# Performance work log

Hardware: AMD Instinct MI355X
Metric: run time of the kernel (lower is better)

The kernel has to match this reference:

```python
import jax, jax.numpy as jnp
import numpy as np

NUM_GROUPS = 32
NUM_HEADS = 8
EPS = 1e-6


def group_norm(x, gamma, beta):
    B, C, H, W = x.shape
    xg = x.reshape(B, NUM_GROUPS, C // NUM_GROUPS, H, W)
    mean = xg.mean(axis=(2, 3, 4), keepdims=True)
    var = xg.var(axis=(2, 3, 4), keepdims=True)
    xn = (xg - mean) * jax.lax.rsqrt(var + EPS)
    xn = xn.reshape(B, C, H, W)
    return xn * gamma[None, :, None, None] + beta[None, :, None, None]


def setup_inputs() -> dict:
    key = jax.random.key(0)
    ks = jax.random.split(key, 3)
    B, C, H, W = 8, 512, 32, 32
    x = jax.random.normal(ks[0], (B, C, H, W), dtype=jnp.float32)
    # xavier_uniform for conv1x1: fan_in=C, fan_out per weight
    lim_qkv = float(np.sqrt(6.0 / (C + 3 * C)))
    w_qkv = jax.random.uniform(ks[1], (3 * C, C), minval=-lim_qkv, maxval=lim_qkv, dtype=jnp.float32)
    b_qkv = jnp.zeros((3 * C,), dtype=jnp.float32)
    lim_p = float(np.sqrt(6.0 / (C + C)))
    w_proj = jax.random.uniform(ks[2], (C, C), minval=-lim_p, maxval=lim_p, dtype=jnp.float32)
    b_proj = jnp.zeros((C,), dtype=jnp.float32)
    gamma = jnp.ones((C,), dtype=jnp.float32)
    beta = jnp.zeros((C,), dtype=jnp.float32)
    return {"x": x, "gamma": gamma, "beta": beta, "w_qkv": w_qkv, "b_qkv": b_qkv,
            "w_proj": w_proj, "b_proj": b_proj}


def reference(x, gamma, beta, w_qkv, b_qkv, w_proj, b_proj):
    B, C, H, W = x.shape
    N = H * W
    hd = C // NUM_HEADS
    scale = hd ** -0.5

    x_norm = group_norm(x, gamma, beta)
    # conv1x1 == channel GEMM: (B,C,H,W) -> (B,3C,H,W)
    qkv = jnp.einsum('bchw,oc->bohw', x_norm, w_qkv) + b_qkv[None, :, None, None]
    qkv = qkv.reshape(B, 3, NUM_HEADS, hd, N).transpose(1, 0, 2, 4, 3)
    q, k, v = qkv[0], qkv[1], qkv[2]

    attn = jnp.einsum('bhnd,bhmd->bhnm', q, k) * scale
    attn = jax.nn.softmax(attn, axis=-1)
    out = jnp.einsum('bhnm,bhmd->bhnd', attn, v)

    out = out.transpose(0, 1, 3, 2).reshape(B, C, H, W)
    out = jnp.einsum('bchw,oc->bohw', out, w_proj) + b_proj[None, :, None, None]
    return x + out
```

## Files before the change

### kernel.cpp

```cpp
#include <hip/hip_runtime.h>

#define LOG2E 1.4426950408889634f

typedef short bf16x8 __attribute__((ext_vector_type(8)));
typedef short short4v __attribute__((ext_vector_type(4)));
typedef float f32x4 __attribute__((ext_vector_type(4)));
typedef _Float16 half4v __attribute__((ext_vector_type(4)));
typedef unsigned u32x4 __attribute__((ext_vector_type(4)));
typedef unsigned __attribute__((address_space(1))) u32g;
typedef unsigned __attribute__((address_space(3))) u32l;

#define MFMA16(a, b, c) __builtin_amdgcn_mfma_f32_16x16x32_bf16((a), (b), (c), 0, 0, 0)

__device__ __forceinline__ short f2bf(float f) {
  unsigned u = __builtin_bit_cast(unsigned, f);
  u += 0x7FFFu + ((u >> 16) & 1u);
  return (short)(u >> 16);
}

__device__ __forceinline__ unsigned cvtpk(float lo, float hi) {
  unsigned r;
  asm("v_cvt_pk_bf16_f32 %0, %1, %2" : "=v"(r) : "v"(lo), "v"(hi));
  return r;
}

__device__ __forceinline__ void g2l16(void* lds, const void* g) {
  __builtin_amdgcn_global_load_lds((u32g*)const_cast<void*>(g), (u32l*)lds, 16, 0, 0);
}

__global__ __launch_bounds__(256) void gn_kernel(const float* __restrict__ x,
                                                 const float* __restrict__ gamma,
                                                 const float* __restrict__ beta,
                                                 short* __restrict__ xn_t) {
  __shared__ _Float16 xs[16 * 1024];
  __shared__ float red[8];
  const int bg = blockIdx.x;
  const int b = bg >> 5, g = bg & 31;
  const int t = threadIdx.x;
  const float4* gx4 = (const float4*)(x + (size_t)(b * 512 + g * 16) * 1024);
  float s1 = 0.f, s2 = 0.f;
  for (int i = 0; i < 16; ++i) {
    float4 v = gx4[t + 256 * i];
    s1 += (v.x + v.y) + (v.z + v.w);
    s2 += (v.x * v.x + v.y * v.y) + (v.z * v.z + v.w * v.w);
    half4v pk = {(_Float16)v.x, (_Float16)v.y, (_Float16)v.z, (_Float16)v.w};
    *(half4v*)((char*)xs + i * 2048 + ((8 * t) ^ ((i & 7) << 4))) = pk;
  }
  for (int m = 1; m < 64; m <<= 1) {
    s1 += __shfl_xor(s1, m);
    s2 += __shfl_xor(s2, m);
  }
  if ((t & 63) == 0) {
    red[(t >> 6) * 2] = s1;
    red[(t >> 6) * 2 + 1] = s2;
  }
  __syncthreads();
  s1 = (red[0] + red[2]) + (red[4] + red[6]);
  s2 = (red[1] + red[3]) + (red[5] + red[7]);
  const float mean = s1 * (1.f / 16384.f);
  const float var = s2 * (1.f / 16384.f) - mean * mean;
  const float rstd = rsqrtf(var + 1e-6f);
  const int ci = t & 15;
  const float ga = gamma[g * 16 + ci] * rstd;
  const float be = beta[g * 16 + ci] - mean * ga;
  short* dst = xn_t + (size_t)b * 1024 * 512 + g * 16 + ci;
  const int sw = (ci & 7) << 4;
  for (int i = 0; i < 64; ++i) {
    int n = (t >> 4) + 16 * i;
    float v = (float)*(const _Float16*)((const char*)xs + ci * 2048 + ((2 * n) ^ sw));
    dst[(size_t)n * 512] = f2bf(fmaf(v, ga, be));
  }
}

__global__ __launch_bounds__(256) void f2bf2_kernel(const float* __restrict__ s1,
                                                    short* __restrict__ d1, int n1,
                                                    const float* __restrict__ s2,
                                                    short* __restrict__ d2) {
  int i = blockIdx.x * 256 + threadIdx.x;
  const float* s = (i < n1) ? s1 : s2;
  short* d = (i < n1) ? d1 : d2;
  int j = (i < n1) ? i : i - n1;
  float4 v = ((const float4*)s)[j];
  short4v o = {f2bf(v.x), f2bf(v.y), f2bf(v.z), f2bf(v.w)};
  *(short4v*)(d + (size_t)j * 4) = o;
}

__global__ __launch_bounds__(512, 6) void qkv_gemm(const short* __restrict__ W,
                                                   const short* __restrict__ xn,
                                                   const float* __restrict__ bias,
                                                   short* __restrict__ qbuf,
                                                   short* __restrict__ kbuf,
                                                   short* __restrict__ vtbuf) {
  __shared__ short a_sm[3][128 * 32];
  __shared__ short b_sm[3][128 * 32];
  const int t = threadIdx.x;
  const int lane = t & 63, w = t >> 6;
  const int nbase = blockIdx.x * 128;
  const int mbase = blockIdx.y * 128;
  const int b = blockIdx.z;
  const short* Asrc = W + (size_t)mbase * 512;
  const short* Bsrc = xn + (size_t)b * 1024 * 512 + (size_t)nbase * 512;

  const int j = t;
  const int r = j >> 2, c = ((j & 3) ^ ((j >> 3) & 3)) * 8;

#define STAGE(bi, kt)                                              \
  {                                                                \
    const int k0s = (kt) * 32;                                     \
    g2l16(&a_sm[bi][j * 8], Asrc + (size_t)r * 512 + k0s + c);     \
    g2l16(&b_sm[bi][j * 8], Bsrc + (size_t)r * 512 + k0s + c);     \
  }

  const int wm = (w >> 2) * 64, wn = (w & 3) * 32;
  const int col = lane & 15, rg = lane >> 4;

  f32x4 acc[4][2] = {};

  STAGE(0, 0)
  STAGE(1, 1)

  for (int kt = 0; kt < 16; ++kt) {
    const int cur = kt % 3;
    if (kt < 15) {
      asm volatile("s_waitcnt vmcnt(2)" ::: "memory");
    } else {
      asm volatile("s_waitcnt vmcnt(0)" ::: "memory");
    }
    __builtin_amdgcn_s_barrier();
    __builtin_amdgcn_sched_barrier(0);
    if (kt < 14) STAGE((kt + 2) % 3, kt + 2)

    bf16x8 af[4], bfr[2];
#pragma unroll
    for (int mf = 0; mf < 4; ++mf) {
      const int row = wm + mf * 16 + col;
      af[mf] = *(const bf16x8*)&a_sm[cur][row * 32 + ((rg ^ ((row >> 1) & 3)) * 8)];
    }
#pragma unroll
    for (int nf = 0; nf < 2; ++nf) {
      const int row = wn + nf * 16 + col;
      bfr[nf] = *(const bf16x8*)&b_sm[cur][row * 32 + ((rg ^ ((row >> 1) & 3)) * 8)];
    }
    __builtin_amdgcn_s_setprio(1);
#pragma unroll
    for (int mf = 0; mf < 4; ++mf)
#pragma unroll
      for (int nf = 0; nf < 2; ++nf)
        acc[mf][nf] = MFMA16(af[mf], bfr[nf], acc[mf][nf]);
    __builtin_amdgcn_s_setprio(0);
  }
#undef STAGE

  __syncthreads();
  short* e_sm = (short*)a_sm;
  const int section = mbase >> 9;
  const int bh0 = b * 8 + ((mbase >> 6) & 7);

  if (section < 2) {
#pragma unroll
    for (int mf = 0; mf < 4; ++mf) {
      const int o0 = mbase + wm + mf * 16 + rg * 4;
      float b4[4];
#pragma unroll
      for (int r2 = 0; r2 < 4; ++r2) b4[r2] = bias[o0 + r2];
      const int mloc0 = wm + mf * 16 + rg * 4;
#pragma unroll
      for (int nf = 0; nf < 2; ++nf) {
        const int nn = wn + nf * 16 + col;
#pragma unroll
        for (int r2 = 0; r2 < 4; ++r2) {
          const int m = mloc0 + r2;
          e_sm[nn * 128 + (((m >> 3) ^ (nn & 7)) << 3) + (m & 7)] =
              f2bf(acc[mf][nf][r2] + b4[r2]);
        }
      }
    }
    __syncthreads();
    short* dst = (section == 0) ? qbuf : kbuf;
#pragma unroll
    for (int p = 0; p < 4; ++p) {
      const int idx = p * 512 + t;
      const int kd = idx & 7, rr = idx >> 3;
      const int hh = rr >> 7, nn = rr & 127;
      const int cm = hh * 8 + kd;
      uint4 vvv = *(const uint4*)&e_sm[nn * 128 + ((cm ^ (nn & 7)) << 3)];
      *(uint4*)&dst[((size_t)(bh0 + hh) * 1024 + nbase + nn) * 64 + kd * 8] = vvv;
    }
  } else {
#pragma unroll
    for (int mf = 0; mf < 4; ++mf) {
      const int o0 = mbase + wm + mf * 16 + rg * 4;
      float b4[4];
#pragma unroll
      for (int r2 = 0; r2 < 4; ++r2) b4[r2] = bias[o0 + r2];
      const int mloc0 = wm + mf * 16 + rg * 4;
#pragma unroll
      for (int nf = 0; nf < 2; ++nf) {
        const int nn = wn + nf * 16 + col;
        const int cn = nn >> 3;
#pragma unroll
        for (int r2 = 0; r2 < 4; ++r2) {
          const int m = mloc0 + r2;
          e_sm[m * 128 + ((cn ^ (m & 7)) << 3) + (nn & 7)] =
              f2bf(acc[mf][nf][r2] + b4[r2]);
        }
      }
    }
    __syncthreads();
#pragma unroll
    for (int p = 0; p < 4; ++p) {
      const int idx = p * 512 + t;
      const int kd = idx & 15, m = idx >> 4;
      const int hh = m >> 6, dd = m & 63;
      uint4 vvv = *(const uint4*)&e_sm[m * 128 + ((kd ^ (m & 7)) << 3)];
      *(uint4*)&vtbuf[((size_t)(bh0 + hh) * 64 + dd) * 1024 + nbase + kd * 8] = vvv;
    }
  }
}

__global__ __launch_bounds__(512, 4) void attn_kernel(const short* __restrict__ qbuf,
                                                      const short* __restrict__ kbuf,
                                                      const short* __restrict__ vtbuf,
                                                      short* __restrict__ ao) {
  __shared__ char smem[65536];
  const int t = threadIdx.x, lane = t & 63, w = t >> 6;
  const int col = lane & 15, rg = lane >> 4;
  const int grp = w >> 2, wq = w & 3;
  const int tg = t & 255;
  const int bh = blockIdx.x, qt = blockIdx.y;
  const int b = bh >> 3, h = bh & 7;
  const int qbase = qt * 128 + wq * 32;

  short* kb_ = (short*)(smem + grp * 32768);
  short* vb_ = (short*)(smem + grp * 32768 + 16384);

  bf16x8 aq[2][2];
  {
    const short* qp = qbuf + ((size_t)bh * 1024 + qbase) * 64;
#pragma unroll
    for (int mf = 0; mf < 2; ++mf)
#pragma unroll
      for (int kc = 0; kc < 2; ++kc)
        aq[mf][kc] = *(const bf16x8*)&qp[(mf * 16 + col) * 64 + kc * 32 + rg * 8];
  }

  const short* kp0 = kbuf + (size_t)bh * 65536 + grp * 32768;
  const short* vp0 = vtbuf + (size_t)bh * 65536 + grp * 512;

  uint4 kr[2], vr[2];
#define LOADK(kt)                                                                  \
  _Pragma("unroll") for (int i = 0; i < 2; ++i) {                                  \
    int j = tg + 256 * i;                                                          \
    kr[i] = *(const uint4*)&kp0[((size_t)(kt)*64 + (j >> 3)) * 64 + (j & 7) * 8];  \
  }
#define LOADV(kt)                                                                  \
  _Pragma("unroll") for (int i = 0; i < 2; ++i) {                                  \
    int j = tg + 256 * i;                                                          \
    vr[i] = *(const uint4*)&vp0[(size_t)(j >> 3) * 1024 + (kt)*64 + (j & 7) * 8];  \
  }
#define WRITEK(bi)                                                                 \
  _Pragma("unroll") for (int i = 0; i < 2; ++i) {                                  \
    int j = tg + 256 * i;                                                          \
    int row = j >> 3, off = j & 7;                                                 \
    *(uint4*)((char*)kb_ + (bi)*8192 + row * 128 + ((off * 16) ^ ((row & 7) << 4))) = kr[i]; \
  }
#define WRITEV(bi)                                                                 \
  _Pragma("unroll") for (int i = 0; i < 2; ++i) {                                  \
    int j = tg + 256 * i;                                                          \
    int d = j >> 3, g = j & 7;                                                     \
    int base = (g >> 2) * 64 + (g & 1) * 32 + ((g >> 1) & 1) * 8;                  \
    char* vb = (char*)vb_ + (bi)*8192 + d * 128;                                   \
    uint2 lo = {vr[i].x, vr[i].y}, hi = {vr[i].z, vr[i].w};                        \
    *(uint2*)(vb + ((base) ^ ((d & 7) << 4))) = lo;                                \
    *(uint2*)(vb + ((base + 16) ^ ((d & 7) << 4))) = hi;                           \
  }

  f32x4 oacc[2][4] = {};
  float mrun[2] = {-3e38f, -3e38f}, lrun[2] = {0.f, 0.f};
  const float kSL2E = 0.125f * LOG2E;
  int cur = 0;

  LOADK(0) LOADV(0) WRITEK(0) WRITEV(0)
  __syncthreads();

  for (int kt = 0; kt < 8; ++kt) {
    if (kt < 7) { LOADK(kt + 1) LOADV(kt + 1) }

    f32x4 sT[2][4];
    __builtin_amdgcn_s_setprio(1);
#pragma unroll
    for (int nf = 0; nf < 4; ++nf) {
      const int n = nf * 16 + col;
      const char* kb = (const char*)kb_ + cur * 8192 + n * 128;
      const int sw = (n & 7) << 4;
      bf16x8 bk0 = *(const bf16x8*)(kb + ((rg * 16) ^ sw));
      bf16x8 bk1 = *(const bf16x8*)(kb + ((64 + rg * 16) ^ sw));
#pragma unroll
      for (int mf = 0; mf < 2; ++mf) {
        f32x4 z = {};
        z = MFMA16(bk0, aq[mf][0], z);
        sT[mf][nf] = MFMA16(bk1, aq[mf][1], z);
      }
    }
    __builtin_amdgcn_s_setprio(0);

    unsigned pk[2][4][2];
#pragma unroll
    for (int mf = 0; mf < 2; ++mf) {
      f32x4 mv = sT[mf][0];
#pragma unroll
      for (int nf = 1; nf < 4; ++nf)
#pragma unroll
        for (int r = 0; r < 4; ++r) mv[r] = fmaxf(mv[r], sT[mf][nf][r]);
      float mx = fmaxf(fmaxf(mv[0], mv[1]), fmaxf(mv[2], mv[3]));
      if (!__all(mx * 0.125f <= mrun[mf] + 8.f)) {
        float mxr = fmaxf(mx, __shfl_xor(mx, 16));
        mxr = fmaxf(mxr, __shfl_xor(mxr, 32));
        const float pmax = mxr * 0.125f;
        const float mnew = fmaxf(mrun[mf], pmax);
        const float alpha = __builtin_amdgcn_exp2f((mrun[mf] - mnew) * LOG2E);
        mrun[mf] = mnew;
        lrun[mf] *= alpha;
#pragma unroll
        for (int df = 0; df < 4; ++df) oacc[mf][df] *= alpha;
      }
      const float nege = mrun[mf] * LOG2E;
      float psum = 0.f;
#pragma unroll
      for (int nf = 0; nf < 4; ++nf) {
        float p0 = __builtin_amdgcn_exp2f(fmaf(sT[mf][nf][0], kSL2E, -nege));
        float p1 = __builtin_amdgcn_exp2f(fmaf(sT[mf][nf][1], kSL2E, -nege));
        float p2 = __builtin_amdgcn_exp2f(fmaf(sT[mf][nf][2], kSL2E, -nege));
        float p3 = __builtin_amdgcn_exp2f(fmaf(sT[mf][nf][3], kSL2E, -nege));
        psum += (p0 + p1) + (p2 + p3);
        pk[mf][nf][0] = cvtpk(p0, p1);
        pk[mf][nf][1] = cvtpk(p2, p3);
      }
      lrun[mf] += psum;
    }

    __builtin_amdgcn_s_setprio(1);
#pragma unroll
    for (int kc = 0; kc < 2; ++kc) {
      bf16x8 pb[2];
#pragma unroll
      for (int mf = 0; mf < 2; ++mf) {
        u32x4 pbu = {pk[mf][2 * kc][0], pk[mf][2 * kc][1], pk[mf][2 * kc + 1][0],
                     pk[mf][2 * kc + 1][1]};
        pb[mf] = __builtin_bit_cast(bf16x8, pbu);
      }
#pragma unroll
      for (int df = 0; df < 4; ++df) {
        const int d = df * 16 + col;
        bf16x8 av = *(const bf16x8*)((const char*)vb_ + cur * 8192 + d * 128 +
                                     ((kc * 64 + rg * 16) ^ ((d & 7) << 4)));
#pragma unroll
        for (int mf = 0; mf < 2; ++mf) oacc[mf][df] = MFMA16(av, pb[mf], oacc[mf][df]);
      }
    }
    __builtin_amdgcn_s_setprio(0);

    if (kt < 7) { WRITEK(cur ^ 1) WRITEV(cur ^ 1) }
    __syncthreads();
    cur ^= 1;
  }

#pragma unroll
  for (int mf = 0; mf < 2; ++mf) {
    float l = lrun[mf];
    l += __shfl_xor(l, 16);
    l += __shfl_xor(l, 32);
    lrun[mf] = l;
  }

  f32x4* o_lds = (f32x4*)smem;
  float* ml_lds = (float*)(smem + 32768);
  short* o16 = (short*)(smem + 36864);
  if (grp == 1) {
#pragma unroll
    for (int mf = 0; mf < 2; ++mf) {
#pragma unroll
      for (int df = 0; df < 4; ++df)
        o_lds[(((wq * 2 + mf) * 4) + df) * 64 + lane] = oacc[mf][df];
      ml_lds[((wq * 2 + mf) * 64 + lane) * 2] = mrun[mf];
      ml_lds[((wq * 2 + mf) * 64 + lane) * 2 + 1] = lrun[mf];
    }
  }
  __syncthreads();
  if (grp == 0) {
#pragma unroll
    for (int mf = 0; mf < 2; ++mf) {
      const float m1 = ml_lds[((wq * 2 + mf) * 64 + lane) * 2];
      const float l1 = ml_lds[((wq * 2 + mf) * 64 + lane) * 2 + 1];
      const float m = fmaxf(mrun[mf], m1);
      const float a0 = __builtin_amdgcn_exp2f((mrun[mf] - m) * LOG2E);
      const float a1 = __builtin_amdgcn_exp2f((m1 - m) * LOG2E);
      const float rl = 1.f / (lrun[mf] * a0 + l1 * a1);
      const int qq = wq * 32 + mf * 16 + col;
#pragma unroll
      for (int df = 0; df < 4; ++df) {
        f32x4 o1 = o_lds[(((wq * 2 + mf) * 4) + df) * 64 + lane];
        short4v pkv;
#pragma unroll
        for (int r = 0; r < 4; ++r)
          pkv[r] = f2bf((oacc[mf][df][r] * a0 + o1[r] * a1) * rl);
        const int cd = df * 2 + (rg >> 1);
        *(short4v*)&o16[qq * 64 + ((cd ^ (qq & 7)) << 3) + (rg & 1) * 4] = pkv;
      }
    }
  }
  __syncthreads();
#pragma unroll
  for (int p = 0; p < 2; ++p) {
    const int idx = p * 512 + t;
    const int kd = idx & 7, qq = idx >> 3;
    uint4 vvv = *(const uint4*)&o16[qq * 64 + ((kd ^ (qq & 7)) << 3)];
    *(uint4*)&ao[((size_t)b * 1024 + qt * 128 + qq) * 512 + h * 64 + kd * 8] = vvv;
  }
#undef LOADK
#undef LOADV
#undef WRITEK
#undef WRITEV
}

__global__ __launch_bounds__(256) void proj_gemm(const short* __restrict__ W,
                                                 const short* __restrict__ ao,
                                                 const float* __restrict__ bias,
                                                 const float* __restrict__ x,
                                                 float* __restrict__ out) {
  __shared__ short a_sm[3][64 * 32];
  __shared__ short b_sm[3][128 * 32];
  const int t = threadIdx.x;
  const int lane = t & 63, w = t >> 6;
  const int nbase = blockIdx.x * 128;
  const int mbase = blockIdx.y * 64;
  const int b = blockIdx.z;
  const short* Asrc = W + (size_t)mbase * 512;
  const short* Bsrc = ao + (size_t)b * 1024 * 512 + (size_t)nbase * 512;

  const int j0 = t, j1 = t + 256;
  const int r0 = j0 >> 2, c0 = ((j0 & 3) ^ ((j0 >> 3) & 3)) * 8;
  const int r1 = j1 >> 2, c1 = ((j1 & 3) ^ ((j1 >> 3) & 3)) * 8;

#define STAGE(bi, kt)                                                 \
  {                                                                   \
    const int k0s = (kt) * 32;                                        \
    g2l16(&a_sm[bi][j0 * 8], Asrc + (size_t)r0 * 512 + k0s + c0);     \
    g2l16(&b_sm[bi][j0 * 8], Bsrc + (size_t)r0 * 512 + k0s + c0);     \
    g2l16(&b_sm[bi][j1 * 8], Bsrc + (size_t)r1 * 512 + k0s + c1);     \
  }

  const int wm = (w >> 1) * 32, wn = (w & 1) * 64;
  const int col = lane & 15, rg = lane >> 4;

  f32x4 acc[2][4] = {};

  STAGE(0, 0)
  STAGE(1, 1)

  for (int kt = 0; kt < 16; ++kt) {
    const int cur = kt % 3;
    if (kt < 15) {
      asm volatile("s_waitcnt vmcnt(3)" ::: "memory");
    } else {
      asm volatile("s_waitcnt vmcnt(0)" ::: "memory");
    }
    __builtin_amdgcn_s_barrier();
    __builtin_amdgcn_sched_barrier(0);
    if (kt < 14) STAGE((kt + 2) % 3, kt + 2)

    bf16x8 af[2], bfr[4];
#pragma unroll
    for (int mf = 0; mf < 2; ++mf) {
      const int row = wm + mf * 16 + col;
      af[mf] = *(const bf16x8*)&a_sm[cur][row * 32 + ((rg ^ ((row >> 1) & 3)) * 8)];
    }
#pragma unroll
    for (int nf = 0; nf < 4; ++nf) {
      const int row = wn + nf * 16 + col;
      bfr[nf] = *(const bf16x8*)&b_sm[cur][row * 32 + ((rg ^ ((row >> 1) & 3)) * 8)];
    }
    __builtin_amdgcn_s_setprio(1);
#pragma unroll
    for (int mf = 0; mf < 2; ++mf)
#pragma unroll
      for (int nf = 0; nf < 4; ++nf)
        acc[mf][nf] = MFMA16(af[mf], bfr[nf], acc[mf][nf]);
    __builtin_amdgcn_s_setprio(0);
  }
#undef STAGE

  for (int mf = 0; mf < 2; ++mf) {
    const int o0 = mbase + wm + mf * 16 + rg * 4;
    float b4[4];
    for (int r = 0; r < 4; ++r) b4[r] = bias[o0 + r];
    for (int nf = 0; nf < 4; ++nf) {
      const int n = nbase + wn + nf * 16 + col;
      for (int r = 0; r < 4; ++r) {
        size_t idx = ((size_t)b * 512 + o0 + r) * 1024 + n;
        out[idx] = x[idx] + acc[mf][nf][r] + b4[r];
      }
    }
  }
}

extern "C" void kernel_launch(void* const* d_in, const int* in_sizes, int n_in,
                              void* d_out, int out_size, void* d_ws, size_t ws_size,
                              hipStream_t stream) {
  const float* x = (const float*)d_in[0];
  const float* gamma = (const float*)d_in[1];
  const float* beta = (const float*)d_in[2];
  const float* w_qkv = (const float*)d_in[3];
  const float* b_qkv = (const float*)d_in[4];
  const float* w_proj = (const float*)d_in[5];
  const float* b_proj = (const float*)d_in[6];
  float* out = (float*)d_out;

  char* ws = (char*)d_ws;
  short* xn_t = (short*)(ws);
  short* wqkv_b = (short*)(ws + 8388608);
  short* wproj_b = (short*)(ws + 9961472);
  short* qbuf = (short*)(ws + 10485760);
  short* kbuf = (short*)(ws + 18874368);
  short* vtbuf = (short*)(ws + 27262976);
  short* aobuf = (short*)(ws + 35651584);

  gn_kernel<<<dim3(256), dim3(256), 0, stream>>>(x, gamma, beta, xn_t);
  f2bf2_kernel<<<dim3(1024), dim3(256), 0, stream>>>(w_qkv, wqkv_b, 196608, w_proj,
                                                     wproj_b);
  qkv_gemm<<<dim3(8, 12, 8), dim3(512), 0, stream>>>(wqkv_b, xn_t, b_qkv, qbuf, kbuf,
                                                     vtbuf);
  attn_kernel<<<dim3(64, 8), dim3(512), 0, stream>>>(qbuf, kbuf, vtbuf, aobuf);
  proj_gemm<<<dim3(8, 8, 8), dim3(256), 0, stream>>>(wproj_b, aobuf, b_proj, x, out);
}
```

Measured before the change: 73.01 us.

## Fuse group-norm apply into QKV GEMM, loading fp32 x directly into B fragments

The group-norm kernel now only computes per-channel scale and shift. The QKV GEMM reads fp32 x directly, applies the normalization in registers, packs to bf16 and feeds the MFMA B operand without staging B in LDS. This removes the transposed bf16 xn_t write and re-read and the separate normalize pass. In exchange, each of the 12 M-tile blocks rereads fp32 x from global memory, using strided scalar loads, and occupancy drops (launch bounds 6 to 4).

Result: slower. 89.96 us (+23.2%).

```diff
diff --git a/kernel.cpp b/kernel.cpp
--- a/kernel.cpp
+++ b/kernel.cpp
@@ -5,7 +5,6 @@
 typedef short bf16x8 __attribute__((ext_vector_type(8)));
 typedef short short4v __attribute__((ext_vector_type(4)));
 typedef float f32x4 __attribute__((ext_vector_type(4)));
-typedef _Float16 half4v __attribute__((ext_vector_type(4)));
 typedef unsigned u32x4 __attribute__((ext_vector_type(4)));
 typedef unsigned __attribute__((address_space(1))) u32g;
 typedef unsigned __attribute__((address_space(3))) u32l;
@@ -28,11 +27,11 @@
   __builtin_amdgcn_global_load_lds((u32g*)const_cast<void*>(g), (u32l*)lds, 16, 0, 0);
 }
 
-__global__ __launch_bounds__(256) void gn_kernel(const float* __restrict__ x,
-                                                 const float* __restrict__ gamma,
-                                                 const float* __restrict__ beta,
-                                                 short* __restrict__ xn_t) {
-  __shared__ _Float16 xs[16 * 1024];
+__global__ __launch_bounds__(256) void gn_stats(const float* __restrict__ x,
+                                                const float* __restrict__ gamma,
+                                                const float* __restrict__ beta,
+                                                float* __restrict__ sa,
+                                                float* __restrict__ sb) {
   __shared__ float red[8];
   const int bg = blockIdx.x;
   const int b = bg >> 5, g = bg & 31;
@@ -43,8 +42,6 @@
     float4 v = gx4[t + 256 * i];
     s1 += (v.x + v.y) + (v.z + v.w);
     s2 += (v.x * v.x + v.y * v.y) + (v.z * v.z + v.w * v.w);
-    half4v pk = {(_Float16)v.x, (_Float16)v.y, (_Float16)v.z, (_Float16)v.w};
-    *(half4v*)((char*)xs + i * 2048 + ((8 * t) ^ ((i & 7) << 4))) = pk;
   }
   for (int m = 1; m < 64; m <<= 1) {
     s1 += __shfl_xor(s1, m);
@@ -60,15 +57,11 @@
   const float mean = s1 * (1.f / 16384.f);
   const float var = s2 * (1.f / 16384.f) - mean * mean;
   const float rstd = rsqrtf(var + 1e-6f);
-  const int ci = t & 15;
-  const float ga = gamma[g * 16 + ci] * rstd;
-  const float be = beta[g * 16 + ci] - mean * ga;
-  short* dst = xn_t + (size_t)b * 1024 * 512 + g * 16 + ci;
-  const int sw = (ci & 7) << 4;
-  for (int i = 0; i < 64; ++i) {
-    int n = (t >> 4) + 16 * i;
-    float v = (float)*(const _Float16*)((const char*)xs + ci * 2048 + ((2 * n) ^ sw));
-    dst[(size_t)n * 512] = f2bf(fmaf(v, ga, be));
+  if (t < 16) {
+    const int c = g * 16 + t;
+    const float ga = gamma[c] * rstd;
+    sa[b * 512 + c] = ga;
+    sb[b * 512 + c] = fmaf(-mean, ga, beta[c]);
   }
 }
 
@@ -85,74 +78,111 @@
   *(short4v*)(d + (size_t)j * 4) = o;
 }
 
-__global__ __launch_bounds__(512, 6) void qkv_gemm(const short* __restrict__ W,
-                                                   const short* __restrict__ xn,
-                                                   const float* __restrict__ bias,
-                                                   short* __restrict__ qbuf,
-                                                   short* __restrict__ kbuf,
-                                                   short* __restrict__ vtbuf) {
-  __shared__ short a_sm[3][128 * 32];
-  __shared__ short b_sm[3][128 * 32];
+__global__ __launch_bounds__(512, 4) void qkv_fused(const float* __restrict__ x,
+                                                    const float* __restrict__ sa,
+                                                    const float* __restrict__ sb,
+                                                    const short* __restrict__ W,
+                                                    const float* __restrict__ bias,
+                                                    short* __restrict__ qbuf,
+                                                    short* __restrict__ kbuf,
+                                                    short* __restrict__ vtbuf) {
+  __shared__ short smem[16384];
+  short (*a_sm)[4096] = (short(*)[4096])smem;
   const int t = threadIdx.x;
   const int lane = t & 63, w = t >> 6;
   const int nbase = blockIdx.x * 128;
   const int mbase = blockIdx.y * 128;
   const int b = blockIdx.z;
   const short* Asrc = W + (size_t)mbase * 512;
-  const short* Bsrc = xn + (size_t)b * 1024 * 512 + (size_t)nbase * 512;
-
-  const int j = t;
-  const int r = j >> 2, c = ((j & 3) ^ ((j >> 3) & 3)) * 8;
-
-#define STAGE(bi, kt)                                              \
-  {                                                                \
-    const int k0s = (kt) * 32;                                     \
-    g2l16(&a_sm[bi][j * 8], Asrc + (size_t)r * 512 + k0s + c);     \
-    g2l16(&b_sm[bi][j * 8], Bsrc + (size_t)r * 512 + k0s + c);     \
-  }
+  const float* xb = x + (size_t)b * 524288;
+  const float* sap = sa + b * 512;
+  const float* sbp = sb + b * 512;
+
+#define ASTAGE(bi, kt)                                                      \
+  g2l16(&a_sm[bi][t * 8],                                                   \
+        Asrc + (size_t)(t >> 2) * 512 + (kt) * 32 + (((t & 3) ^ ((t >> 3) & 3)) * 8));
 
   const int wm = (w >> 2) * 64, wn = (w & 3) * 32;
   const int col = lane & 15, rg = lane >> 4;
-
+  const int cc = rg;
+  const int n0 = wn + col, n1 = n0 + 16;
+
+  float br0[8], br1[8];
+  float4 s_a0, s_a1, s_b0, s_b1;
+  bf16x8 bfr[2][2];
   f32x4 acc[4][2] = {};
 
-  STAGE(0, 0)
-  STAGE(1, 1)
-
+#define BLOADS(kt)                                                          \
+  {                                                                         \
+    const int kc0 = (kt) * 32 + cc * 8;                                     \
+    _Pragma("unroll") for (int e = 0; e < 8; ++e) {                         \
+      br0[e] = xb[(size_t)(kc0 + e) * 1024 + nbase + n0];                   \
+      br1[e] = xb[(size_t)(kc0 + e) * 1024 + nbase + n1];                   \
+    }                                                                       \
+    s_a0 = *(const float4*)&sap[kc0];                                       \
+    s_a1 = *(const float4*)&sap[kc0 + 4];                                   \
+    s_b0 = *(const float4*)&sbp[kc0];                                       \
+    s_b1 = *(const float4*)&sbp[kc0 + 4];                                   \
+  }
+
+#define BUILD(slot)                                                         \
+  {                                                                         \
+    float av[8] = {s_a0.x, s_a0.y, s_a0.z, s_a0.w, s_a1.x, s_a1.y, s_a1.z, s_a1.w}; \
+    float bv[8] = {s_b0.x, s_b0.y, s_b0.z, s_b0.w, s_b1.x, s_b1.y, s_b1.z, s_b1.w}; \
+    u32x4 u0, u1;                                                           \
+    _Pragma("unroll") for (int p = 0; p < 4; ++p) {                         \
+      u0[p] = cvtpk(fmaf(br0[2 * p], av[2 * p], bv[2 * p]),                 \
+                    fmaf(br0[2 * p + 1], av[2 * p + 1], bv[2 * p + 1]));    \
+      u1[p] = cvtpk(fmaf(br1[2 * p], av[2 * p], bv[2 * p]),                 \
+                    fmaf(br1[2 * p + 1], av[2 * p + 1], bv[2 * p + 1]));    \
+    }                                                                       \
+    bfr[slot][0] = __builtin_bit_cast(bf16x8, u0);                          \
+    bfr[slot][1] = __builtin_bit_cast(bf16x8, u1);                          \
+  }
+
+  BLOADS(0)
+  ASTAGE(0, 0)
+  ASTAGE(1, 1)
+  asm volatile("s_waitcnt vmcnt(0)" ::: "memory");
+  BUILD(0)
+  __builtin_amdgcn_s_barrier();
+
+#pragma unroll
   for (int kt = 0; kt < 16; ++kt) {
     const int cur = kt % 3;
-    if (kt < 15) {
-      asm volatile("s_waitcnt vmcnt(2)" ::: "memory");
-    } else {
-      asm volatile("s_waitcnt vmcnt(0)" ::: "memory");
-    }
-    __builtin_amdgcn_s_barrier();
-    __builtin_amdgcn_sched_barrier(0);
-    if (kt < 14) STAGE((kt + 2) % 3, kt + 2)
-
-    bf16x8 af[4], bfr[2];
+    if (kt < 15) BLOADS(kt + 1)
+    if (kt < 14) ASTAGE((kt + 2) % 3, kt + 2)
+
+    bf16x8 af[4];
 #pragma unroll
     for (int mf = 0; mf < 4; ++mf) {
       const int row = wm + mf * 16 + col;
       af[mf] = *(const bf16x8*)&a_sm[cur][row * 32 + ((rg ^ ((row >> 1) & 3)) * 8)];
     }
-#pragma unroll
-    for (int nf = 0; nf < 2; ++nf) {
-      const int row = wn + nf * 16 + col;
-      bfr[nf] = *(const bf16x8*)&b_sm[cur][row * 32 + ((rg ^ ((row >> 1) & 3)) * 8)];
-    }
     __builtin_amdgcn_s_setprio(1);
 #pragma unroll
     for (int mf = 0; mf < 4; ++mf)
 #pragma unroll
       for (int nf = 0; nf < 2; ++nf)
-        acc[mf][nf] = MFMA16(af[mf], bfr[nf], acc[mf][nf]);
+        acc[mf][nf] = MFMA16(af[mf], bfr[kt & 1][nf], acc[mf][nf]);
     __builtin_amdgcn_s_setprio(0);
-  }
-#undef STAGE
+
+    if (kt < 15) {
+      if (kt < 14) {
+        asm volatile("s_waitcnt vmcnt(1)" ::: "memory");
+      } else {
+        asm volatile("s_waitcnt vmcnt(0)" ::: "memory");
+      }
+      BUILD((kt + 1) & 1)
+    }
+    __builtin_amdgcn_s_barrier();
+  }
+#undef ASTAGE
+#undef BLOADS
+#undef BUILD
 
   __syncthreads();
-  short* e_sm = (short*)a_sm;
+  short* e_sm = smem;
   const int section = mbase >> 9;
   const int bh0 = b * 8 + ((mbase >> 6) & 7);
 
@@ -517,7 +547,8 @@
   float* out = (float*)d_out;
 
   char* ws = (char*)d_ws;
-  short* xn_t = (short*)(ws);
+  float* sa = (float*)(ws);
+  float* sb = (float*)(ws + 16384);
   short* wqkv_b = (short*)(ws + 8388608);
   short* wproj_b = (short*)(ws + 9961472);
   short* qbuf = (short*)(ws + 10485760);
@@ -525,11 +556,11 @@
   short* vtbuf = (short*)(ws + 27262976);
   short* aobuf = (short*)(ws + 35651584);
 
-  gn_kernel<<<dim3(256), dim3(256), 0, stream>>>(x, gamma, beta, xn_t);
+  gn_stats<<<dim3(256), dim3(256), 0, stream>>>(x, gamma, beta, sa, sb);
   f2bf2_kernel<<<dim3(1024), dim3(256), 0, stream>>>(w_qkv, wqkv_b, 196608, w_proj,
                                                      wproj_b);
-  qkv_gemm<<<dim3(8, 12, 8), dim3(512), 0, stream>>>(wqkv_b, xn_t, b_qkv, qbuf, kbuf,
-                                                     vtbuf);
+  qkv_fused<<<dim3(8, 12, 8), dim3(512), 0, stream>>>(x, sa, sb, wqkv_b, b_qkv, qbuf,
+                                                      kbuf, vtbuf);
   attn_kernel<<<dim3(64, 8), dim3(512), 0, stream>>>(qbuf, kbuf, vtbuf, aobuf);
   proj_gemm<<<dim3(8, 8, 8), dim3(256), 0, stream>>>(wproj_b, aobuf, b_proj, x, out);
 }
```

## Split attention KV into four groups with smaller query tiles and single-buffered LDS

Applied to the files above, without the earlier changes.

The attention kernel now processes 64 queries per block instead of 128 and splits the key/value sequence across four warp groups instead of two. The grid doubles to 1024 blocks and LDS use drops from 64KB to about 38KB. The partial results are merged with a two-level tree reduction through shared memory. Double buffering of K/V tiles is replaced by one buffer per group with an extra barrier each iteration. The intent is more blocks per CU and better occupancy, at the cost of less overlap between loads and compute and more merge overhead.

Measured after the change: 228.4 us. 213% more time.

```diff
diff --git a/kernel.cpp b/kernel.cpp
--- a/kernel.cpp
+++ b/kernel.cpp
@@ -218,21 +218,21 @@
   }
 }
 
-__global__ __launch_bounds__(512, 4) void attn_kernel(const short* __restrict__ qbuf,
+__global__ __launch_bounds__(512, 6) void attn_kernel(const short* __restrict__ qbuf,
                                                       const short* __restrict__ kbuf,
                                                       const short* __restrict__ vtbuf,
                                                       short* __restrict__ ao) {
-  __shared__ char smem[65536];
+  __shared__ char smem[38912];
   const int t = threadIdx.x, lane = t & 63, w = t >> 6;
   const int col = lane & 15, rg = lane >> 4;
-  const int grp = w >> 2, wq = w & 3;
-  const int tg = t & 255;
+  const int grp = w >> 1, wq = w & 1;
+  const int tg = t & 127;
   const int bh = blockIdx.x, qt = blockIdx.y;
   const int b = bh >> 3, h = bh & 7;
-  const int qbase = qt * 128 + wq * 32;
-
-  short* kb_ = (short*)(smem + grp * 32768);
-  short* vb_ = (short*)(smem + grp * 32768 + 16384);
+  const int qbase = qt * 64 + wq * 32;
+
+  char* kbase = smem + grp * 8192;
+  char* vbase = smem + grp * 8192 + 4096;
 
   bf16x8 aq[2][2];
   {
@@ -244,54 +244,54 @@
         aq[mf][kc] = *(const bf16x8*)&qp[(mf * 16 + col) * 64 + kc * 32 + rg * 8];
   }
 
-  const short* kp0 = kbuf + (size_t)bh * 65536 + grp * 32768;
-  const short* vp0 = vtbuf + (size_t)bh * 65536 + grp * 512;
+  const short* kp0 = kbuf + (size_t)bh * 65536 + grp * 16384;
+  const short* vp0 = vtbuf + (size_t)bh * 65536 + grp * 256;
 
   uint4 kr[2], vr[2];
-#define LOADK(kt)                                                                  \
-  _Pragma("unroll") for (int i = 0; i < 2; ++i) {                                  \
-    int j = tg + 256 * i;                                                          \
-    kr[i] = *(const uint4*)&kp0[((size_t)(kt)*64 + (j >> 3)) * 64 + (j & 7) * 8];  \
-  }
-#define LOADV(kt)                                                                  \
-  _Pragma("unroll") for (int i = 0; i < 2; ++i) {                                  \
-    int j = tg + 256 * i;                                                          \
-    vr[i] = *(const uint4*)&vp0[(size_t)(j >> 3) * 1024 + (kt)*64 + (j & 7) * 8];  \
-  }
-#define WRITEK(bi)                                                                 \
-  _Pragma("unroll") for (int i = 0; i < 2; ++i) {                                  \
-    int j = tg + 256 * i;                                                          \
-    int row = j >> 3, off = j & 7;                                                 \
-    *(uint4*)((char*)kb_ + (bi)*8192 + row * 128 + ((off * 16) ^ ((row & 7) << 4))) = kr[i]; \
-  }
-#define WRITEV(bi)                                                                 \
-  _Pragma("unroll") for (int i = 0; i < 2; ++i) {                                  \
-    int j = tg + 256 * i;                                                          \
-    int d = j >> 3, g = j & 7;                                                     \
-    int base = (g >> 2) * 64 + (g & 1) * 32 + ((g >> 1) & 1) * 8;                  \
-    char* vb = (char*)vb_ + (bi)*8192 + d * 128;                                   \
-    uint2 lo = {vr[i].x, vr[i].y}, hi = {vr[i].z, vr[i].w};                        \
-    *(uint2*)(vb + ((base) ^ ((d & 7) << 4))) = lo;                                \
-    *(uint2*)(vb + ((base + 16) ^ ((d & 7) << 4))) = hi;                           \
+#define LOADK(kt)                                                                 \
+  _Pragma("unroll") for (int i = 0; i < 2; ++i) {                                 \
+    int j = tg + 128 * i;                                                         \
+    kr[i] = *(const uint4*)&kp0[(kt)*2048 + (j >> 3) * 64 + (j & 7) * 8];         \
+  }
+#define LOADV(kt)                                                                 \
+  _Pragma("unroll") for (int i = 0; i < 2; ++i) {                                 \
+    int j = tg + 128 * i;                                                         \
+    vr[i] = *(const uint4*)&vp0[(size_t)(j >> 2) * 1024 + (kt)*32 + (j & 3) * 8]; \
+  }
+#define WRITEK()                                                                  \
+  _Pragma("unroll") for (int i = 0; i < 2; ++i) {                                 \
+    int j = tg + 128 * i;                                                         \
+    int row = j >> 3, off = j & 7;                                                \
+    *(uint4*)(kbase + row * 128 + ((off * 16) ^ ((row & 7) << 4))) = kr[i];       \
+  }
+#define WRITEV()                                                                  \
+  _Pragma("unroll") for (int i = 0; i < 2; ++i) {                                 \
+    int j = tg + 128 * i;                                                         \
+    int d = j >> 2, g4 = j & 3;                                                   \
+    int vrow = d >> 1;                                                            \
+    int base = (d & 1) * 64 + (g4 & 1) * 32 + (g4 >> 1) * 8;                      \
+    int sw = (vrow & 7) << 4;                                                     \
+    uint2 lo = {vr[i].x, vr[i].y}, hi = {vr[i].z, vr[i].w};                       \
+    *(uint2*)(vbase + vrow * 128 + (base ^ sw)) = lo;                             \
+    *(uint2*)(vbase + vrow * 128 + ((base + 16) ^ sw)) = hi;                      \
   }
 
   f32x4 oacc[2][4] = {};
   float mrun[2] = {-3e38f, -3e38f}, lrun[2] = {0.f, 0.f};
   const float kSL2E = 0.125f * LOG2E;
-  int cur = 0;
-
-  LOADK(0) LOADV(0) WRITEK(0) WRITEV(0)
+
+  LOADK(0) LOADV(0) WRITEK() WRITEV()
   __syncthreads();
 
   for (int kt = 0; kt < 8; ++kt) {
     if (kt < 7) { LOADK(kt + 1) LOADV(kt + 1) }
 
-    f32x4 sT[2][4];
+    f32x4 sT[2][2];
     __builtin_amdgcn_s_setprio(1);
 #pragma unroll
-    for (int nf = 0; nf < 4; ++nf) {
+    for (int nf = 0; nf < 2; ++nf) {
       const int n = nf * 16 + col;
-      const char* kb = (const char*)kb_ + cur * 8192 + n * 128;
+      const char* kb = kbase + n * 128;
       const int sw = (n & 7) << 4;
       bf16x8 bk0 = *(const bf16x8*)(kb + ((rg * 16) ^ sw));
       bf16x8 bk1 = *(const bf16x8*)(kb + ((64 + rg * 16) ^ sw));
@@ -304,14 +304,12 @@
     }
     __builtin_amdgcn_s_setprio(0);
 
-    unsigned pk[2][4][2];
+    unsigned pk[2][2][2];
 #pragma unroll
     for (int mf = 0; mf < 2; ++mf) {
       f32x4 mv = sT[mf][0];
 #pragma unroll
-      for (int nf = 1; nf < 4; ++nf)
-#pragma unroll
-        for (int r = 0; r < 4; ++r) mv[r] = fmaxf(mv[r], sT[mf][nf][r]);
+      for (int r = 0; r < 4; ++r) mv[r] = fmaxf(mv[r], sT[mf][1][r]);
       float mx = fmaxf(fmaxf(mv[0], mv[1]), fmaxf(mv[2], mv[3]));
       if (!__all(mx * 0.125f <= mrun[mf] + 8.f)) {
         float mxr = fmaxf(mx, __shfl_xor(mx, 16));
@@ -327,7 +325,7 @@
       const float nege = mrun[mf] * LOG2E;
       float psum = 0.f;
 #pragma unroll
-      for (int nf = 0; nf < 4; ++nf) {
+      for (int nf = 0; nf < 2; ++nf) {
         float p0 = __builtin_amdgcn_exp2f(fmaf(sT[mf][nf][0], kSL2E, -nege));
         float p1 = __builtin_amdgcn_exp2f(fmaf(sT[mf][nf][1], kSL2E, -nege));
         float p2 = __builtin_amdgcn_exp2f(fmaf(sT[mf][nf][2], kSL2E, -nege));
@@ -340,29 +338,28 @@
     }
 
     __builtin_amdgcn_s_setprio(1);
-#pragma unroll
-    for (int kc = 0; kc < 2; ++kc) {
+    {
       bf16x8 pb[2];
 #pragma unroll
       for (int mf = 0; mf < 2; ++mf) {
-        u32x4 pbu = {pk[mf][2 * kc][0], pk[mf][2 * kc][1], pk[mf][2 * kc + 1][0],
-                     pk[mf][2 * kc + 1][1]};
+        u32x4 pbu = {pk[mf][0][0], pk[mf][0][1], pk[mf][1][0], pk[mf][1][1]};
         pb[mf] = __builtin_bit_cast(bf16x8, pbu);
       }
 #pragma unroll
       for (int df = 0; df < 4; ++df) {
         const int d = df * 16 + col;
-        bf16x8 av = *(const bf16x8*)((const char*)vb_ + cur * 8192 + d * 128 +
-                                     ((kc * 64 + rg * 16) ^ ((d & 7) << 4)));
+        const int vrow = d >> 1;
+        bf16x8 av = *(const bf16x8*)(vbase + vrow * 128 +
+                                     (((d & 1) * 64 + rg * 16) ^ ((vrow & 7) << 4)));
 #pragma unroll
         for (int mf = 0; mf < 2; ++mf) oacc[mf][df] = MFMA16(av, pb[mf], oacc[mf][df]);
       }
     }
     __builtin_amdgcn_s_setprio(0);
 
-    if (kt < 7) { WRITEK(cur ^ 1) WRITEV(cur ^ 1) }
     __syncthreads();
-    cur ^= 1;
+    if (kt < 7) { WRITEK() WRITEV() }
+    __syncthreads();
   }
 
 #pragma unroll
@@ -373,54 +370,72 @@
     lrun[mf] = l;
   }
 
-  f32x4* o_lds = (f32x4*)smem;
-  float* ml_lds = (float*)(smem + 32768);
-  short* o16 = (short*)(smem + 36864);
-  if (grp == 1) {
+  f32x4* slotA = (f32x4*)smem;
+  f32x4* slotB = (f32x4*)(smem + 16384);
+  float* ml1 = (float*)(smem + 32768);
+  float* ml3 = (float*)(smem + 34816);
+  float* ml2 = (float*)(smem + 36864);
+  short* o16 = (short*)(smem + 16384);
+
+#define DUMP(slot, ml)                                                        \
+  _Pragma("unroll") for (int mf = 0; mf < 2; ++mf) {                          \
+    _Pragma("unroll") for (int df = 0; df < 4; ++df)                          \
+        slot[(((wq * 2 + mf) * 4) + df) * 64 + lane] = oacc[mf][df];          \
+    ml[((wq * 2 + mf) * 64 + lane) * 2] = mrun[mf];                           \
+    ml[((wq * 2 + mf) * 64 + lane) * 2 + 1] = lrun[mf];                       \
+  }
+#define MERGE(slot, ml)                                                       \
+  _Pragma("unroll") for (int mf = 0; mf < 2; ++mf) {                          \
+    const float m1 = ml[((wq * 2 + mf) * 64 + lane) * 2];                     \
+    const float l1 = ml[((wq * 2 + mf) * 64 + lane) * 2 + 1];                 \
+    const float m = fmaxf(mrun[mf], m1);                                      \
+    const float a0 = __builtin_amdgcn_exp2f((mrun[mf] - m) * LOG2E);          \
+    const float a1 = __builtin_amdgcn_exp2f((m1 - m) * LOG2E);                \
+    mrun[mf] = m;                                                             \
+    lrun[mf] = lrun[mf] * a0 + l1 * a1;                                       \
+    _Pragma("unroll") for (int df = 0; df < 4; ++df) {                        \
+      f32x4 o1 = slot[(((wq * 2 + mf) * 4) + df) * 64 + lane];                \
+      _Pragma("unroll") for (int r = 0; r < 4; ++r)                           \
+          oacc[mf][df][r] = oacc[mf][df][r] * a0 + o1[r] * a1;                \
+    }                                                                         \
+  }
+
+  if (grp == 1) { DUMP(slotA, ml1) }
+  if (grp == 3) { DUMP(slotB, ml3) }
+  __syncthreads();
+  if (grp == 0) { MERGE(slotA, ml1) }
+  if (grp == 2) { MERGE(slotB, ml3) }
+  __syncthreads();
+  if (grp == 2) { DUMP(slotA, ml2) }
+  __syncthreads();
+  if (grp == 0) {
+    MERGE(slotA, ml2)
 #pragma unroll
     for (int mf = 0; mf < 2; ++mf) {
-#pragma unroll
-      for (int df = 0; df < 4; ++df)
-        o_lds[(((wq * 2 + mf) * 4) + df) * 64 + lane] = oacc[mf][df];
-      ml_lds[((wq * 2 + mf) * 64 + lane) * 2] = mrun[mf];
-      ml_lds[((wq * 2 + mf) * 64 + lane) * 2 + 1] = lrun[mf];
-    }
-  }
-  __syncthreads();
-  if (grp == 0) {
-#pragma unroll
-    for (int mf = 0; mf < 2; ++mf) {
-      const float m1 = ml_lds[((wq * 2 + mf) * 64 + lane) * 2];
-      const float l1 = ml_lds[((wq * 2 + mf) * 64 + lane) * 2 + 1];
-      const float m = fmaxf(mrun[mf], m1);
-      const float a0 = __builtin_amdgcn_exp2f((mrun[mf] - m) * LOG2E);
-      const float a1 = __builtin_amdgcn_exp2f((m1 - m) * LOG2E);
-      const float rl = 1.f / (lrun[mf] * a0 + l1 * a1);
+      const float rl = 1.f / lrun[mf];
       const int qq = wq * 32 + mf * 16 + col;
 #pragma unroll
       for (int df = 0; df < 4; ++df) {
-        f32x4 o1 = o_lds[(((wq * 2 + mf) * 4) + df) * 64 + lane];
         short4v pkv;
 #pragma unroll
-        for (int r = 0; r < 4; ++r)
-          pkv[r] = f2bf((oacc[mf][df][r] * a0 + o1[r] * a1) * rl);
+        for (int r = 0; r < 4; ++r) pkv[r] = f2bf(oacc[mf][df][r] * rl);
         const int cd = df * 2 + (rg >> 1);
         *(short4v*)&o16[qq * 64 + ((cd ^ (qq & 7)) << 3) + (rg & 1) * 4] = pkv;
       }
     }
   }
   __syncthreads();
-#pragma unroll
-  for (int p = 0; p < 2; ++p) {
-    const int idx = p * 512 + t;
-    const int kd = idx & 7, qq = idx >> 3;
+  {
+    const int kd = t & 7, qq = t >> 3;
     uint4 vvv = *(const uint4*)&o16[qq * 64 + ((kd ^ (qq & 7)) << 3)];
-    *(uint4*)&ao[((size_t)b * 1024 + qt * 128 + qq) * 512 + h * 64 + kd * 8] = vvv;
+    *(uint4*)&ao[((size_t)b * 1024 + qt * 64 + qq) * 512 + h * 64 + kd * 8] = vvv;
   }
 #undef LOADK
 #undef LOADV
 #undef WRITEK
 #undef WRITEV
+#undef DUMP
+#undef MERGE
 }
 
 __global__ __launch_bounds__(256) void proj_gemm(const short* __restrict__ W,
@@ -530,6 +545,6 @@
                                                      wproj_b);
   qkv_gemm<<<dim3(8, 12, 8), dim3(512), 0, stream>>>(wqkv_b, xn_t, b_qkv, qbuf, kbuf,
                                                      vtbuf);
-  attn_kernel<<<dim3(64, 8), dim3(512), 0, stream>>>(qbuf, kbuf, vtbuf, aobuf);
+  attn_kernel<<<dim3(64, 16), dim3(512), 0, stream>>>(qbuf, kbuf, vtbuf, aobuf);
   proj_gemm<<<dim3(8, 8, 8), dim3(256), 0, stream>>>(wproj_b, aobuf, b_proj, x, out);
 }
```
